# Kernel tuning notes

Hardware: AMD Instinct MI355X
Metric: run time of the kernel (lower is better)

The kernel has to match this reference:

```python
import jax, jax.numpy as jnp
import numpy as np

H = 4  # num_heads in all three MultiheadAttention layers


def _mha(x, valid, Wq, Wk, Wv, Wo, bq, bk, bv, bo):
    """Batched self-attention with key_padding_mask, matching torch MHA math.
    x: [..., L, D]; valid: [..., L] float (1=real token, 0=pad)."""
    lead = x.shape[:-2]
    L, D = x.shape[-2], x.shape[-1]
    dh = D // H
    q = (x @ Wq + bq).reshape(*lead, L, H, dh)
    k = (x @ Wk + bk).reshape(*lead, L, H, dh)
    v = (x @ Wv + bv).reshape(*lead, L, H, dh)
    scores = jnp.einsum('...qhd,...khd->...hqk', q, k) / jnp.sqrt(jnp.asarray(dh, x.dtype))
    neg = jnp.asarray(-1e9, x.dtype)  # finite so fully-masked rows stay NaN-free
    scores = jnp.where(valid[..., None, None, :] > 0, scores, neg)
    a = jax.nn.softmax(scores, axis=-1)
    o = jnp.einsum('...hqk,...khd->...qhd', a, v).reshape(*lead, L, D)
    return o @ Wo + bo


def _masked_mean(x, m):
    # (x * m).sum over sequence / (m.sum + 1e-10); fully-masked -> exact zeros,
    # matching the torch zeros() fallback branch.
    mm = m[..., None]
    return (x * mm).sum(-2) / (mm.sum(-2) + 1e-10)


def setup_inputs() -> dict:
    key = jax.random.key(0)
    B, S, N, W, D = 16, 8, 16, 64, 256
    ks = jax.random.split(key, 16)
    inp = {
        'word_embeddings': jax.random.normal(ks[0], (B, S, N, W, D), dtype=jnp.float32),
        'attention_mask': jax.random.randint(ks[1], (B, S, N, W), 0, 2).astype(jnp.int32),
    }
    i = 2
    for lvl in 'wsc':  # word / sentence / section attention params
        for p in ('Wq', 'Wk', 'Wv', 'Wo'):
            inp[lvl + p] = 0.02 * jax.random.normal(ks[i], (D, D), dtype=jnp.float32)
            i += 1
        for p in ('bq', 'bk', 'bv', 'bo'):
            inp[lvl + p] = jnp.zeros((D,), jnp.float32)
    return inp


def reference(word_embeddings, attention_mask,
              wWq, wWk, wWv, wWo, wbq, wbk, wbv, wbo,
              sWq, sWk, sWv, sWo, sbq, sbk, sbv, sbo,
              cWq, cWk, cWv, cWo, cbq, cbk, cbv, cbo):
    dt = word_embeddings.dtype
    mask = attention_mask.astype(dt)                       # [B,S,N,W]
    # word level: attention within each sentence, then masked mean pooling
    wo = _mha(word_embeddings, mask, wWq, wWk, wWv, wWo, wbq, wbk, wbv, wbo)
    sent = _masked_mean(wo, mask)                          # [B,S,N,D]
    # sentence level
    sent_mask = (mask.sum(-1) > 0).astype(dt)              # [B,S,N]
    so = _mha(sent, sent_mask, sWq, sWk, sWv, sWo, sbq, sbk, sbv, sbo)
    sec = _masked_mean(so, sent_mask)                      # [B,S,D]
    # section level
    sec_mask = (mask.sum((-1, -2)) > 0).astype(dt)         # [B,S]
    co = _mha(sec, sec_mask, cWq, cWk, cWv, cWo, cbq, cbk, cbv, cbo)
    doc = _masked_mean(co, sec_mask)                       # [B,D]
    return doc
```

## Files before the change

### kernel.cpp

```cpp
#include <hip/hip_runtime.h>

constexpr int D = 256;

typedef __attribute__((ext_vector_type(8))) __bf16 bf16x8;
typedef __attribute__((ext_vector_type(4))) float f32x4;

__device__ inline unsigned short f2b(float f) {
    unsigned u = __builtin_bit_cast(unsigned, f);
    u = (u + 0x7fffu + ((u >> 16) & 1u)) >> 16;
    return (unsigned short)u;
}
__device__ inline unsigned cvt_pk_bf16(float lo, float hi) {
    unsigned r;
    asm volatile("v_cvt_pk_bf16_f32 %0, %1, %2" : "=v"(r) : "v"(lo), "v"(hi));
    return r;
}
__device__ inline bf16x8 ld_frag(const void* p) {
    uint4 r = *(const uint4*)p;
    return __builtin_bit_cast(bf16x8, r);
}

__global__ void prep_wt3(const float* __restrict__ q0, const float* __restrict__ k0,
                         const float* __restrict__ q1, const float* __restrict__ k1,
                         const float* __restrict__ q2, const float* __restrict__ k2,
                         unsigned short* __restrict__ WT) {
    const int b = blockIdx.x, k = threadIdx.x;
    const int lvl = b >> 9, c = b & 511;
    const float* Wq = (lvl == 0) ? q0 : (lvl == 1) ? q1 : q2;
    const float* Wk = (lvl == 0) ? k0 : (lvl == 1) ? k1 : k2;
    const float* W = (c < 256) ? Wq : Wk;
    WT[(size_t)b * 256 + k] = f2b(W[k * 256 + (c & 255)]);
}

template<int NSUB, typename MT>
__global__ __launch_bounds__(512, 4)
void attn_kernel(const float* __restrict__ X, const MT* __restrict__ Mask,
                 const unsigned short* __restrict__ WT,
                 const float* __restrict__ bq, const float* __restrict__ bk,
                 const float* __restrict__ Wv, const float* __restrict__ Wo,
                 const float* __restrict__ bv, const float* __restrict__ bo,
                 float* __restrict__ Out0, float* __restrict__ Out1)
{
    constexpr int LSUB = 64 / NSUB;
    constexpr int L2S  = (LSUB == 64) ? 6 : (LSUB == 16) ? 4 : 3;
    constexpr int NS   = (NSUB > 1) ? NSUB : 1;

    __shared__ unsigned short sQK[64 * 512];
    __shared__ float sM[64];
    __shared__ float sPart[8][64];
    __shared__ float sCt[NS];
    __shared__ float sAbarT[64][4];
    __shared__ float sAbar[4][64];
    __shared__ float sPP[NS][256];
    __shared__ float sH[2][NS][256];

    const int tid = threadIdx.x;
    const int blk = blockIdx.x;
    const float* Xs = X + (size_t)blk * 64 * D;
    char* sB = (char*)sQK;
    const int lane = tid & 63, w = tid >> 6;
    const int lr = lane & 15, lg = lane >> 4;

    uint2 pk[8];
    {
        const float4* X4 = (const float4*)Xs;
        float4 xv[8];
        #pragma unroll
        for (int j = 0; j < 8; ++j) xv[j] = X4[tid + j * 512];
        if (tid < 64) sM[tid] = (float)Mask[(size_t)blk * 64 + tid];
        #pragma unroll
        for (int j = 0; j < 8; ++j) {
            pk[j].x = cvt_pk_bf16(xv[j].x, xv[j].y);
            pk[j].y = cvt_pk_bf16(xv[j].z, xv[j].w);
            const int row = w + 8 * j;
            *(uint2*)(sB + row * 512 + ((lane * 8) ^ ((row & 7) << 4))) = pk[j];
        }
    }
    __syncthreads();
    if (tid < 64) {
        float v = sM[tid];
        #pragma unroll
        for (int o = 1; o < LSUB; o <<= 1) v += __shfl_xor(v, o);
        if ((tid & (LSUB - 1)) == 0) sCt[tid >> L2S] = v;
    }

    f32x4 acc[4][4];
    {
        const float* bias = (w < 4) ? bq : bk;
        const int fb = (w & 3) * 64;
        #pragma unroll
        for (int m = 0; m < 4; ++m) {
            float4 b4 = *(const float4*)(bias + fb + m * 16 + lg * 4);
            f32x4 bi = {b4.x, b4.y, b4.z, b4.w};
            #pragma unroll
            for (int n = 0; n < 4; ++n) acc[m][n] = bi;
        }
        const unsigned short* wtp = WT + (size_t)(w * 64 + lr) * 256 + lg * 8;
        bf16x8 afn[4];
        #pragma unroll
        for (int m = 0; m < 4; ++m) afn[m] = ld_frag(wtp + m * 16 * 256);
        #pragma unroll 1
        for (int kk = 0; kk < 8; ++kk) {
            bf16x8 af[4];
            #pragma unroll
            for (int m = 0; m < 4; ++m) af[m] = afn[m];
            if (kk < 7) {
                #pragma unroll
                for (int m = 0; m < 4; ++m) afn[m] = ld_frag(wtp + m * 16 * 256 + (kk + 1) * 32);
            }
            bf16x8 bx[4];
            #pragma unroll
            for (int n = 0; n < 4; ++n) {
                int t = n * 16 + lr;
                bx[n] = ld_frag(sB + t * 512 + ((kk * 64 + lg * 16) ^ ((t & 7) << 4)));
            }
            __builtin_amdgcn_s_setprio(1);
            #pragma unroll
            for (int m = 0; m < 4; ++m)
                #pragma unroll
                for (int n = 0; n < 4; ++n)
                    acc[m][n] = __builtin_amdgcn_mfma_f32_16x16x32_bf16(af[m], bx[n], acc[m][n], 0, 0, 0);
            __builtin_amdgcn_s_setprio(0);
        }
    }
    __syncthreads();
    #pragma unroll
    for (int n = 0; n < 4; ++n) {
        int t = n * 16 + lr;
        char* rowp = sB + t * 1024;
        int sw = (t & 7) << 4;
        #pragma unroll
        for (int m = 0; m < 4; ++m) {
            uint2 qk;
            qk.x = cvt_pk_bf16(acc[m][n][0], acc[m][n][1]);
            qk.y = cvt_pk_bf16(acc[m][n][2], acc[m][n][3]);
            *(uint2*)(rowp + ((w * 128 + m * 32 + lg * 8) ^ sw)) = qk;
        }
    }
    __syncthreads();

    {
        const int h = w >> 1, msel = w & 1;
        f32x4 sacc[2][4];
        #pragma unroll
        for (int m = 0; m < 2; ++m)
            #pragma unroll
            for (int n = 0; n < 4; ++n) sacc[m][n] = (f32x4){0.f, 0.f, 0.f, 0.f};
        #pragma unroll
        for (int kk = 0; kk < 2; ++kk) {
            bf16x8 qf[2];
            #pragma unroll
            for (int m = 0; m < 2; ++m) {
                int t = msel * 32 + m * 16 + lr;
                qf[m] = ld_frag(sB + t * 1024 + ((h * 128 + kk * 64 + lg * 16) ^ ((t & 7) << 4)));
            }
            #pragma unroll
            for (int n = 0; n < 4; ++n) {
                int t = n * 16 + lr;
                bf16x8 kf = ld_frag(sB + t * 1024 + ((512 + h * 128 + kk * 64 + lg * 16) ^ ((t & 7) << 4)));
                #pragma unroll
                for (int m = 0; m < 2; ++m)
                    sacc[m][n] = __builtin_amdgcn_mfma_f32_16x16x32_bf16(qf[m], kf, sacc[m][n], 0, 0, 0);
            }
        }
        float mcol[4];
        int csub[4];
        #pragma unroll
        for (int n = 0; n < 4; ++n) {
            mcol[n] = sM[n * 16 + lr];
            csub[n] = (n * 16 + lr) >> L2S;
        }
        constexpr float CE = 0.125f * 1.44269504f;
        float pm[4] = {0.f, 0.f, 0.f, 0.f};
        #pragma unroll
        for (int m = 0; m < 2; ++m)
            #pragma unroll
            for (int r = 0; r < 4; ++r) {
                const int rowtok = msel * 32 + m * 16 + lg * 4 + r;
                const int rsub = rowtok >> L2S;
                float s[4], mx = -3.4e38f;
                #pragma unroll
                for (int n = 0; n < 4; ++n) {
                    float v = sacc[m][n][r];
                    bool ok = (mcol[n] > 0.f);
                    if constexpr (NSUB > 1) ok = ok && (csub[n] == rsub);
                    v = ok ? v : -1e9f;
                    s[n] = v; mx = fmaxf(mx, v);
                }
                #pragma unroll
                for (int o = 1; o < 16; o <<= 1) mx = fmaxf(mx, __shfl_xor(mx, o));
                float e[4], se = 0.f;
                #pragma unroll
                for (int n = 0; n < 4; ++n) { e[n] = exp2f((s[n] - mx) * CE); se += e[n]; }
                #pragma unroll
                for (int o = 1; o < 16; o <<= 1) se += __shfl_xor(se, o);
                const float wr = sM[rowtok] / se;
                #pragma unroll
                for (int n = 0; n < 4; ++n) pm[n] += e[n] * wr;
            }
        #pragma unroll
        for (int o = 16; o < 64; o <<= 1)
            #pragma unroll
            for (int n = 0; n < 4; ++n) pm[n] += __shfl_xor(pm[n], o);
        if (lane < 16)
            #pragma unroll
            for (int n = 0; n < 4; ++n) sPart[w][n * 16 + lane] = pm[n];
    }
    __syncthreads();

    if constexpr (NSUB == 1) {
        if (tid < 256) {
            int h = tid >> 6, j = tid & 63;
            sAbarT[j][h] = sPart[2 * h][j] + sPart[2 * h + 1][j];
        }
        __syncthreads();
        float zp[4][4];
        #pragma unroll
        for (int h = 0; h < 4; ++h)
            #pragma unroll
            for (int e = 0; e < 4; ++e) zp[h][e] = 0.f;
        #pragma unroll
        for (int j = 0; j < 8; ++j) {
            const int t = w + 8 * j;
            f32x4 ab = *(const f32x4*)&sAbarT[t][0];
            float x0 = __builtin_bit_cast(float, pk[j].x << 16);
            float x1 = __builtin_bit_cast(float, pk[j].x & 0xffff0000u);
            float x2 = __builtin_bit_cast(float, pk[j].y << 16);
            float x3 = __builtin_bit_cast(float, pk[j].y & 0xffff0000u);
            #pragma unroll
            for (int h = 0; h < 4; ++h) {
                zp[h][0] = fmaf(ab[h], x0, zp[h][0]);
                zp[h][1] = fmaf(ab[h], x1, zp[h][1]);
                zp[h][2] = fmaf(ab[h], x2, zp[h][2]);
                zp[h][3] = fmaf(ab[h], x3, zp[h][3]);
            }
        }
        #pragma unroll
        for (int h = 0; h < 4; ++h) {
            const int slot = (h + (lane >> 2)) & 3;
            *(f32x4*)(sB + (size_t)(w * 64 + lane) * 64 + slot * 16) =
                (f32x4){zp[h][0], zp[h][1], zp[h][2], zp[h][3]};
        }
        __syncthreads();
        {
            const int d = tid & 255, hp = (tid >> 8) * 2;
            const int ln = d >> 2, e = d & 3;
            const int s0_ = (hp + (ln >> 2)) & 3;
            const int s1_ = (hp + 1 + (ln >> 2)) & 3;
            float a0 = 0.f, a1 = 0.f;
            #pragma unroll
            for (int ww = 0; ww < 8; ++ww) {
                const float* pb = (const float*)(sB + (size_t)(ww * 64 + ln) * 64);
                a0 += pb[s0_ * 4 + e];
                a1 += pb[s1_ * 4 + e];
            }
            float* Zo = Out0 + (size_t)blk * 1024;
            Zo[hp * 256 + d] = a0;
            Zo[(hp + 1) * 256 + d] = a1;
        }
        if (tid == 0) Out1[blk] = sCt[0];
    } else {
        if (tid < 256) {
            int h = tid >> 6, j = tid & 63;
            sAbar[h][j] = sPart[2 * h][j] + sPart[2 * h + 1][j];
        }
        __syncthreads();
        float* zpf = (float*)sB;
        const int d = tid & 255, rh = tid >> 8;
        constexpr int HT = LSUB / 2;
        #pragma unroll
        for (int s = 0; s < NSUB; ++s) {
            float zz[4] = {0.f, 0.f, 0.f, 0.f};
            const int t0 = s * LSUB + rh * HT;
            #pragma unroll
            for (int t = 0; t < HT; ++t) {
                float xv = Xs[(size_t)(t0 + t) * 256 + d];
                #pragma unroll
                for (int h = 0; h < 4; ++h) zz[h] = fmaf(sAbar[h][t0 + t], xv, zz[h]);
            }
            #pragma unroll
            for (int h = 0; h < 4; ++h) zpf[((rh * NSUB + s) * 4 + h) * 256 + d] = zz[h];
        }
        __syncthreads();
        {
            const int n = tid & 255, g = tid >> 8, h = n >> 6;
            float pa[NSUB];
            #pragma unroll
            for (int s = 0; s < NSUB; ++s) pa[s] = 0.f;
            for (int dc = 0; dc < 128; dc += 8) {
                float wv[8];
                #pragma unroll
                for (int q = 0; q < 8; ++q) wv[q] = Wv[(size_t)(g * 128 + dc + q) * 256 + n];
                #pragma unroll
                for (int s = 0; s < NSUB; ++s)
                    #pragma unroll
                    for (int q = 0; q < 8; ++q) {
                        int dd = g * 128 + dc + q;
                        float zv = zpf[(s * 4 + h) * 256 + dd] + zpf[((NSUB + s) * 4 + h) * 256 + dd];
                        pa[s] = fmaf(zv, wv[q], pa[s]);
                    }
            }
            #pragma unroll
            for (int s = 0; s < NSUB; ++s) sH[g][s][n] = pa[s];
        }
        __syncthreads();
        for (int i = tid; i < NSUB * 256; i += 512) {
            int s = i >> 8, nn = i & 255;
            sPP[s][nn] = sH[0][s][nn] + sH[1][s][nn] + sCt[s] * bv[nn];
        }
        __syncthreads();
        {
            const int n = tid & 255, g = tid >> 8;
            float pa[NSUB];
            #pragma unroll
            for (int s = 0; s < NSUB; ++s) pa[s] = 0.f;
            for (int dc = 0; dc < 128; dc += 8) {
                float wo[8];
                #pragma unroll
                for (int q = 0; q < 8; ++q) wo[q] = Wo[(size_t)(g * 128 + dc + q) * 256 + n];
                #pragma unroll
                for (int s = 0; s < NSUB; ++s) {
                    const float* pp = &sPP[s][g * 128 + dc];
                    #pragma unroll
                    for (int q = 0; q < 8; ++q) pa[s] = fmaf(pp[q], wo[q], pa[s]);
                }
            }
            #pragma unroll
            for (int s = 0; s < NSUB; ++s) sH[g][s][n] = pa[s];
        }
        __syncthreads();
        for (int i = tid; i < NSUB * 256; i += 512) {
            int s = i >> 8, nn = i & 255;
            float c = sCt[s];
            Out0[(size_t)(blk * NSUB + s) * 256 + nn] =
                (c > 0.f) ? ((sH[0][s][nn] + sH[1][s][nn]) / c + bo[nn]) : 0.f;
        }
        if (tid < NSUB && Out1) Out1[blk * NSUB + tid] = (sCt[tid] > 0.f) ? 1.f : 0.f;
    }
}

__global__ __launch_bounds__(512, 4)
void apply2(const float* __restrict__ Z, const float* __restrict__ Cnt,
            const float* __restrict__ Wv, const float* __restrict__ Wo,
            const float* __restrict__ bv, const float* __restrict__ bo,
            float* __restrict__ Out, float* __restrict__ MaskOut)
{
    constexpr int SPB = 4;
    __shared__ float sZ[SPB][4][256];
    __shared__ float sPP[SPB][256];
    __shared__ float sH[2][SPB][256];
    __shared__ float sCt[SPB];

    const int tid = threadIdx.x;
    const int s0 = blockIdx.x * SPB;
    {
        const float4* Zf = (const float4*)(Z + (size_t)s0 * 1024);
        float4* sZf = (float4*)sZ;
        #pragma unroll
        for (int k = 0; k < 2; ++k) sZf[tid + k * 512] = Zf[tid + k * 512];
        if (tid < SPB) sCt[tid] = Cnt[s0 + tid];
    }
    __syncthreads();

    const int n = tid & 255, g = tid >> 8, h = n >> 6;

    {
        float pa[SPB] = {0.f, 0.f, 0.f, 0.f};
        for (int dc = 0; dc < 128; dc += 16) {
            float wv[16];
            #pragma unroll
            for (int q = 0; q < 16; ++q) wv[q] = Wv[(size_t)(g * 128 + dc + q) * 256 + n];
            #pragma unroll
            for (int s = 0; s < SPB; ++s) {
                const float4* zp4 = (const float4*)&sZ[s][h][g * 128 + dc];
                #pragma unroll
                for (int q4 = 0; q4 < 4; ++q4) {
                    float4 zv = zp4[q4];
                    pa[s] = fmaf(zv.x, wv[q4 * 4 + 0], pa[s]);
                    pa[s] = fmaf(zv.y, wv[q4 * 4 + 1], pa[s]);
                    pa[s] = fmaf(zv.z, wv[q4 * 4 + 2], pa[s]);
                    pa[s] = fmaf(zv.w, wv[q4 * 4 + 3], pa[s]);
                }
            }
        }
        #pragma unroll
        for (int s = 0; s < SPB; ++s) sH[g][s][n] = pa[s];
    }
    __syncthreads();
    for (int i = tid; i < SPB * 256; i += 512) {
        int s = i >> 8, nn = i & 255;
        sPP[s][nn] = sH[0][s][nn] + sH[1][s][nn] + sCt[s] * bv[nn];
    }
    __syncthreads();
    {
        float pa[SPB] = {0.f, 0.f, 0.f, 0.f};
        for (int dc = 0; dc < 128; dc += 16) {
            float wo[16];
            #pragma unroll
            for (int q = 0; q < 16; ++q) wo[q] = Wo[(size_t)(g * 128 + dc + q) * 256 + n];
            #pragma unroll
            for (int s = 0; s < SPB; ++s) {
                const float4* pp = (const float4*)&sPP[s][g * 128 + dc];
                #pragma unroll
                for (int q4 = 0; q4 < 4; ++q4) {
                    float4 pv = pp[q4];
                    pa[s] = fmaf(pv.x, wo[q4 * 4 + 0], pa[s]);
                    pa[s] = fmaf(pv.y, wo[q4 * 4 + 1], pa[s]);
                    pa[s] = fmaf(pv.z, wo[q4 * 4 + 2], pa[s]);
                    pa[s] = fmaf(pv.w, wo[q4 * 4 + 3], pa[s]);
                }
            }
        }
        #pragma unroll
        for (int s = 0; s < SPB; ++s) sH[g][s][n] = pa[s];
    }
    __syncthreads();
    for (int i = tid; i < SPB * 256; i += 512) {
        int s = i >> 8, nn = i & 255;
        float c = sCt[s];
        Out[(size_t)(s0 + s) * 256 + nn] = (c > 0.f) ? ((sH[0][s][nn] + sH[1][s][nn]) / c + bo[nn]) : 0.f;
    }
    if (tid < SPB && MaskOut) MaskOut[s0 + tid] = (sCt[tid] > 0.f) ? 1.f : 0.f;
}

extern "C" void kernel_launch(void* const* d_in, const int* in_sizes, int n_in,
                              void* d_out, int out_size, void* d_ws, size_t ws_size,
                              hipStream_t stream)
{
    const float* emb  = (const float*)d_in[0];
    const int*  amask = (const int*)d_in[1];
    const float* W[24];
    for (int i = 0; i < 24; ++i) W[i] = (const float*)d_in[2 + i];

    char* ws = (char*)d_ws;
    unsigned short* WT = (unsigned short*)ws;
    float* zbuf  = (float*)(ws + 3 * 256 * 1024);
    float* cnt   = zbuf + 2048 * 1024;
    float* sent  = cnt + 2048;
    float* smask = sent + 2048 * 256;
    float* sec   = smask + 2048;
    float* cmask = sec + 128 * 256;
    float* out   = (float*)d_out;

    prep_wt3<<<dim3(1536), dim3(256), 0, stream>>>(W[0], W[1], W[8], W[9], W[16], W[17], WT);

    attn_kernel<1, int><<<dim3(2048), dim3(512), 0, stream>>>(
        emb, amask, WT, W[4], W[5], nullptr, nullptr, nullptr, nullptr, zbuf, cnt);
    apply2<<<dim3(512), dim3(512), 0, stream>>>(
        zbuf, cnt, W[2], W[3], W[6], W[7], sent, smask);

    attn_kernel<4, float><<<dim3(32), dim3(512), 0, stream>>>(
        sent, smask, WT + 512 * 256, W[12], W[13], W[10], W[11], W[14], W[15], sec, cmask);

    attn_kernel<8, float><<<dim3(2), dim3(512), 0, stream>>>(
        sec, cmask, WT + 2 * 512 * 256, W[20], W[21], W[18], W[19], W[22], W[23], out, nullptr);
}
```

Before: 183.4 us.

## Use DPP row reductions and fast exp/rcp in softmax, retile apply2 and z-reduction

The softmax row max/sum reductions now use DPP row_shr instead of shuffle-xor, with hardware exp2 and rcp replacing the precise versions. MFMA sections get raised wave priority via s_setprio. The head-weight sums are stored in a shared head-major layout for all variants, and the per-wave partial z reduction uses a simpler row-major layout. apply2 now handles 8 sentences per block with half the grid, so each weight load is reused across more sentences at the cost of lower occupancy.

```diff
diff --git a/kernel.cpp b/kernel.cpp
--- a/kernel.cpp
+++ b/kernel.cpp
@@ -18,6 +18,25 @@
 __device__ inline bf16x8 ld_frag(const void* p) {
     uint4 r = *(const uint4*)p;
     return __builtin_bit_cast(bf16x8, r);
+}
+template<int CTRL>
+__device__ inline float dpp_f(float v) {
+    return __builtin_bit_cast(float,
+        __builtin_amdgcn_update_dpp(0, __builtin_bit_cast(int, v), CTRL, 0xf, 0xf, true));
+}
+__device__ inline float rsum16(float v) {
+    v += dpp_f<0x121>(v);
+    v += dpp_f<0x122>(v);
+    v += dpp_f<0x124>(v);
+    v += dpp_f<0x128>(v);
+    return v;
+}
+__device__ inline float rmax16(float v) {
+    v = fmaxf(v, dpp_f<0x121>(v));
+    v = fmaxf(v, dpp_f<0x122>(v));
+    v = fmaxf(v, dpp_f<0x124>(v));
+    v = fmaxf(v, dpp_f<0x128>(v));
+    return v;
 }
 
 __global__ void prep_wt3(const float* __restrict__ q0, const float* __restrict__ k0,
@@ -49,7 +68,6 @@
     __shared__ float sM[64];
     __shared__ float sPart[8][64];
     __shared__ float sCt[NS];
-    __shared__ float sAbarT[64][4];
     __shared__ float sAbar[4][64];
     __shared__ float sPP[NS][256];
     __shared__ float sH[2][NS][256];
@@ -154,6 +172,7 @@
                 int t = msel * 32 + m * 16 + lr;
                 qf[m] = ld_frag(sB + t * 1024 + ((h * 128 + kk * 64 + lg * 16) ^ ((t & 7) << 4)));
             }
+            __builtin_amdgcn_s_setprio(1);
             #pragma unroll
             for (int n = 0; n < 4; ++n) {
                 int t = n * 16 + lr;
@@ -162,6 +181,7 @@
                 for (int m = 0; m < 2; ++m)
                     sacc[m][n] = __builtin_amdgcn_mfma_f32_16x16x32_bf16(qf[m], kf, sacc[m][n], 0, 0, 0);
             }
+            __builtin_amdgcn_s_setprio(0);
         }
         float mcol[4];
         int csub[4];
@@ -187,14 +207,12 @@
                     v = ok ? v : -1e9f;
                     s[n] = v; mx = fmaxf(mx, v);
                 }
-                #pragma unroll
-                for (int o = 1; o < 16; o <<= 1) mx = fmaxf(mx, __shfl_xor(mx, o));
-                float e[4], se = 0.f;
-                #pragma unroll
-                for (int n = 0; n < 4; ++n) { e[n] = exp2f((s[n] - mx) * CE); se += e[n]; }
-                #pragma unroll
-                for (int o = 1; o < 16; o <<= 1) se += __shfl_xor(se, o);
-                const float wr = sM[rowtok] / se;
+                mx = rmax16(mx);
+                float e[4], se;
+                #pragma unroll
+                for (int n = 0; n < 4; ++n) e[n] = __builtin_amdgcn_exp2f((s[n] - mx) * CE);
+                se = rsum16(((e[0] + e[1]) + (e[2] + e[3])));
+                const float wr = sM[rowtok] * __builtin_amdgcn_rcpf(se);
                 #pragma unroll
                 for (int n = 0; n < 4; ++n) pm[n] += e[n] * wr;
             }
@@ -207,13 +225,13 @@
             for (int n = 0; n < 4; ++n) sPart[w][n * 16 + lane] = pm[n];
     }
     __syncthreads();
+    if (tid < 256) {
+        int h = tid >> 6, j = tid & 63;
+        sAbar[h][j] = sPart[2 * h][j] + sPart[2 * h + 1][j];
+    }
+    __syncthreads();
 
     if constexpr (NSUB == 1) {
-        if (tid < 256) {
-            int h = tid >> 6, j = tid & 63;
-            sAbarT[j][h] = sPart[2 * h][j] + sPart[2 * h + 1][j];
-        }
-        __syncthreads();
         float zp[4][4];
         #pragma unroll
         for (int h = 0; h < 4; ++h)
@@ -222,37 +240,34 @@
         #pragma unroll
         for (int j = 0; j < 8; ++j) {
             const int t = w + 8 * j;
-            f32x4 ab = *(const f32x4*)&sAbarT[t][0];
+            float ab0 = sAbar[0][t], ab1 = sAbar[1][t];
+            float ab2 = sAbar[2][t], ab3 = sAbar[3][t];
             float x0 = __builtin_bit_cast(float, pk[j].x << 16);
             float x1 = __builtin_bit_cast(float, pk[j].x & 0xffff0000u);
             float x2 = __builtin_bit_cast(float, pk[j].y << 16);
             float x3 = __builtin_bit_cast(float, pk[j].y & 0xffff0000u);
-            #pragma unroll
-            for (int h = 0; h < 4; ++h) {
-                zp[h][0] = fmaf(ab[h], x0, zp[h][0]);
-                zp[h][1] = fmaf(ab[h], x1, zp[h][1]);
-                zp[h][2] = fmaf(ab[h], x2, zp[h][2]);
-                zp[h][3] = fmaf(ab[h], x3, zp[h][3]);
-            }
-        }
-        #pragma unroll
-        for (int h = 0; h < 4; ++h) {
-            const int slot = (h + (lane >> 2)) & 3;
-            *(f32x4*)(sB + (size_t)(w * 64 + lane) * 64 + slot * 16) =
+            zp[0][0] = fmaf(ab0, x0, zp[0][0]); zp[0][1] = fmaf(ab0, x1, zp[0][1]);
+            zp[0][2] = fmaf(ab0, x2, zp[0][2]); zp[0][3] = fmaf(ab0, x3, zp[0][3]);
+            zp[1][0] = fmaf(ab1, x0, zp[1][0]); zp[1][1] = fmaf(ab1, x1, zp[1][1]);
+            zp[1][2] = fmaf(ab1, x2, zp[1][2]); zp[1][3] = fmaf(ab1, x3, zp[1][3]);
+            zp[2][0] = fmaf(ab2, x0, zp[2][0]); zp[2][1] = fmaf(ab2, x1, zp[2][1]);
+            zp[2][2] = fmaf(ab2, x2, zp[2][2]); zp[2][3] = fmaf(ab2, x3, zp[2][3]);
+            zp[3][0] = fmaf(ab3, x0, zp[3][0]); zp[3][1] = fmaf(ab3, x1, zp[3][1]);
+            zp[3][2] = fmaf(ab3, x2, zp[3][2]); zp[3][3] = fmaf(ab3, x3, zp[3][3]);
+        }
+        float* zr = (float*)sB;
+        #pragma unroll
+        for (int h = 0; h < 4; ++h)
+            *(f32x4*)&zr[(w * 4 + h) * 256 + lane * 4] =
                 (f32x4){zp[h][0], zp[h][1], zp[h][2], zp[h][3]};
-        }
         __syncthreads();
         {
             const int d = tid & 255, hp = (tid >> 8) * 2;
-            const int ln = d >> 2, e = d & 3;
-            const int s0_ = (hp + (ln >> 2)) & 3;
-            const int s1_ = (hp + 1 + (ln >> 2)) & 3;
             float a0 = 0.f, a1 = 0.f;
             #pragma unroll
             for (int ww = 0; ww < 8; ++ww) {
-                const float* pb = (const float*)(sB + (size_t)(ww * 64 + ln) * 64);
-                a0 += pb[s0_ * 4 + e];
-                a1 += pb[s1_ * 4 + e];
+                a0 += zr[(ww * 4 + hp) * 256 + d];
+                a1 += zr[(ww * 4 + hp + 1) * 256 + d];
             }
             float* Zo = Out0 + (size_t)blk * 1024;
             Zo[hp * 256 + d] = a0;
@@ -260,11 +275,6 @@
         }
         if (tid == 0) Out1[blk] = sCt[0];
     } else {
-        if (tid < 256) {
-            int h = tid >> 6, j = tid & 63;
-            sAbar[h][j] = sPart[2 * h][j] + sPart[2 * h + 1][j];
-        }
-        __syncthreads();
         float* zpf = (float*)sB;
         const int d = tid & 255, rh = tid >> 8;
         constexpr int HT = LSUB / 2;
@@ -339,13 +349,13 @@
     }
 }
 
-__global__ __launch_bounds__(512, 4)
+__global__ __launch_bounds__(512, 2)
 void apply2(const float* __restrict__ Z, const float* __restrict__ Cnt,
             const float* __restrict__ Wv, const float* __restrict__ Wo,
             const float* __restrict__ bv, const float* __restrict__ bo,
             float* __restrict__ Out, float* __restrict__ MaskOut)
 {
-    constexpr int SPB = 4;
+    constexpr int SPB = 8;
     __shared__ float sZ[SPB][4][256];
     __shared__ float sPP[SPB][256];
     __shared__ float sH[2][SPB][256];
@@ -357,7 +367,7 @@
         const float4* Zf = (const float4*)(Z + (size_t)s0 * 1024);
         float4* sZf = (float4*)sZ;
         #pragma unroll
-        for (int k = 0; k < 2; ++k) sZf[tid + k * 512] = Zf[tid + k * 512];
+        for (int k = 0; k < 4; ++k) sZf[tid + k * 512] = Zf[tid + k * 512];
         if (tid < SPB) sCt[tid] = Cnt[s0 + tid];
     }
     __syncthreads();
@@ -365,7 +375,7 @@
     const int n = tid & 255, g = tid >> 8, h = n >> 6;
 
     {
-        float pa[SPB] = {0.f, 0.f, 0.f, 0.f};
+        float pa[SPB] = {};
         for (int dc = 0; dc < 128; dc += 16) {
             float wv[16];
             #pragma unroll
@@ -393,7 +403,7 @@
     }
     __syncthreads();
     {
-        float pa[SPB] = {0.f, 0.f, 0.f, 0.f};
+        float pa[SPB] = {};
         for (int dc = 0; dc < 128; dc += 16) {
             float wo[16];
             #pragma unroll
@@ -446,7 +456,7 @@
 
     attn_kernel<1, int><<<dim3(2048), dim3(512), 0, stream>>>(
         emb, amask, WT, W[4], W[5], nullptr, nullptr, nullptr, nullptr, zbuf, cnt);
-    apply2<<<dim3(512), dim3(512), 0, stream>>>(
+    apply2<<<dim3(256), dim3(512), 0, stream>>>(
         zbuf, cnt, W[2], W[3], W[6], W[7], sent, smask);
 
     attn_kernel<4, float><<<dim3(32), dim3(512), 0, stream>>>(
```

Result: faster. 176.5 us (-3.7%).
